# Optimization experiments

Measured on AMD Instinct MI355X. Metric: run time of the kernel, lower is better.

Reference implementation:

```python
import jax, jax.numpy as jnp
import numpy as np

B, T, D_IN, D_H, D_OUT = 32, 2048, 1024, 1024, 1024

def setup_inputs() -> dict:
    key = jax.random.key(0)
    k1, k2, k3, k4, k5 = jax.random.split(key, 5)
    s = jax.random.normal(k1, (B, D_IN), dtype=jnp.float32)
    h = jax.random.normal(k2, (B, T, D_H), dtype=jnp.float32)
    # params (original uses np.random.random, i.e. uniform [0,1); scale kept modest)
    W_a = jax.random.uniform(k3, (D_IN, D_OUT), dtype=jnp.float32)
    U_a = jax.random.uniform(k4, (D_H, D_OUT), dtype=jnp.float32)
    v_a = jax.random.uniform(k5, (D_OUT,), dtype=jnp.float32)
    return {"s": s, "h": h, "W_a": W_a, "U_a": U_a, "v_a": v_a}

def reference(s, h, W_a, U_a, v_a):
    # Bahdanau additive attention:
    # e_bt = v_a . tanh(s W_a + h_t U_a);  a = softmax_t(e);  c_b = sum_t a_bt h_bt
    u_a_h = jnp.einsum('bth,ho->bto', h, U_a)            # [B,T,O]
    w_a_s = jnp.einsum('bi,io->bo', s, W_a)[:, None, :]  # [B,1,O]
    e = jnp.einsum('bto,o->bt', jnp.tanh(w_a_s + u_a_h), v_a)  # [B,T]
    a = jax.nn.softmax(e, axis=-1)                       # [B,T]
    c = jnp.einsum('bt,bth->bh', a, h)                   # [B,H]
    return c
```

## Files before the change

### kernel.cpp

```cpp
#include <hip/hip_runtime.h>
#include <hip/hip_bf16.h>
#include <stdint.h>

#define Bb 32
#define Tt 2048
#define Dd 1024

typedef float    f32x4 __attribute__((ext_vector_type(4)));
typedef _Float16 f16x8 __attribute__((ext_vector_type(8)));
typedef uint32_t u32;

#define WS_E     131072
#define WS_A     393216
#define WS_CP    655360
#define WS_UT    4849664

__device__ __forceinline__ void gll16(const void* g, const void* lds) {
  __builtin_amdgcn_global_load_lds(
      (const __attribute__((address_space(1))) u32*)(uintptr_t)g,
      (__attribute__((address_space(3))) u32*)(uint32_t)(uintptr_t)lds,
      16, 0, 0);
}

__global__ __launch_bounds__(256) void k_ws(const float* __restrict__ s,
                                            const float* __restrict__ W,
                                            float* __restrict__ w_ws) {
  const int b = blockIdx.x >> 2;
  const int o = (blockIdx.x & 3) * 256 + threadIdx.x;
  __shared__ float s_sh[Dd];
#pragma unroll
  for (int j = 0; j < 4; ++j)
    s_sh[threadIdx.x + 256 * j] = s[b * Dd + threadIdx.x + 256 * j];
  __syncthreads();
  float acc = 0.f;
#pragma unroll 8
  for (int i = 0; i < Dd; ++i) acc += s_sh[i] * W[(size_t)i * Dd + o];
  w_ws[b * Dd + o] = acc;
}

__global__ __launch_bounds__(256) void k_ut(const float* __restrict__ U,
                                            uint8_t* __restrict__ U_ts) {
  const int i0 = (blockIdx.x >> 4) * 64;
  const int o0 = (blockIdx.x & 15) * 64;
  __shared__ float tile[64][65];
  const int tx = threadIdx.x & 63;
  const int ty = threadIdx.x >> 6;
#pragma unroll
  for (int jj = 0; jj < 16; ++jj)
    tile[tx][ty + 4 * jj] = U[(size_t)(i0 + ty + 4 * jj) * Dd + o0 + tx];
  __syncthreads();
#pragma unroll
  for (int jj = 0; jj < 16; ++jj) {
    const int o_loc = ty + 4 * jj;
    const int o = o0 + o_loc;
    const int k = i0 + tx;
    const _Float16 hv = (_Float16)tile[o_loc][tx];
    const size_t byte = (size_t)o * 2048 + (((u32)k * 2u) ^ (u32)((o & 7) << 4));
    *(uint16_t*)(U_ts + byte) = *(const uint16_t*)&hv;
  }
}

__global__ __launch_bounds__(256, 2) void k_e(const float* __restrict__ h,
                                              const uint8_t* __restrict__ U_ts,
                                              const float* __restrict__ w_ws,
                                              const float* __restrict__ v_a,
                                              float* __restrict__ e_ws) {
  const int b    = blockIdx.x >> 5;
  const int t0   = (blockIdx.x & 31) << 6;
  const int lane = threadIdx.x & 63;
  const int wv   = threadIdx.x >> 6;

  __shared__ __align__(16) uint8_t ubuf[2][32 * 512];
  __shared__ float w_sh[Dd];
  __shared__ float v_sh[Dd];

#pragma unroll
  for (int j = 0; j < 4; ++j) {
    const int o = threadIdx.x + 256 * j;
    w_sh[o] = w_ws[b * Dd + o];
    v_sh[o] = v_a[o];
  }

  const int trow = t0 + 16 * wv + (lane & 15);
  const int kcol = (lane >> 4) * 8;
  const float* hbase = h + ((size_t)b * Tt + trow) * Dd + kcol;
  f16x8 hreg[32];
#pragma unroll
  for (int ks = 0; ks < 32; ++ks) {
    const f32x4 p0 = *(const f32x4*)(hbase + ks * 32);
    const f32x4 p1 = *(const f32x4*)(hbase + ks * 32 + 4);
    f16x8 r;
    r[0] = (_Float16)p0[0]; r[1] = (_Float16)p0[1];
    r[2] = (_Float16)p0[2]; r[3] = (_Float16)p0[3];
    r[4] = (_Float16)p1[0]; r[5] = (_Float16)p1[1];
    r[6] = (_Float16)p1[2]; r[7] = (_Float16)p1[3];
    hreg[ks] = r;
  }

  auto stage = [&](int c, int buf) {
    const uint8_t* src = U_ts + (size_t)(c >> 2) * (32 * 2048) + (size_t)(c & 3) * 512;
#pragma unroll
    for (int q = 0; q < 4; ++q) {
      const int r0 = 8 * wv + 2 * q;
      gll16(src + (size_t)(r0 + (lane >> 5)) * 2048 + (size_t)(lane & 31) * 16,
            &ubuf[buf][r0 * 512]);
    }
  };

  stage(0, 0);
  __syncthreads();

  float epart = 0.f;
  const int ol0 = lane & 15;
  const int ol1 = ol0 + 16;
  const u32 kb  = (u32)((lane >> 4) * 16);
  const u32 sw  = (u32)((ol0 & 7) << 4);

  for (int ot = 0; ot < 32; ++ot) {
    f32x4 acc0 = {0.f, 0.f, 0.f, 0.f};
    f32x4 acc1 = {0.f, 0.f, 0.f, 0.f};
#pragma unroll
    for (int kc = 0; kc < 4; ++kc) {
      const int c   = ot * 4 + kc;
      const int cur = kc & 1;
      if (c + 1 < 128) stage(c + 1, cur ^ 1);
      const uint8_t* ub = &ubuf[cur][0];
#pragma unroll
      for (int kk = 0; kk < 8; ++kk) {
        const u32 kbyte = (u32)(kk * 64) + kb;
        const f16x8 a0 = *(const f16x8*)(ub + ol0 * 512 + (kbyte ^ sw));
        const f16x8 a1 = *(const f16x8*)(ub + ol1 * 512 + (kbyte ^ sw));
        acc0 = __builtin_amdgcn_mfma_f32_16x16x32_f16(a0, hreg[kc * 8 + kk], acc0, 0, 0, 0);
        acc1 = __builtin_amdgcn_mfma_f32_16x16x32_f16(a1, hreg[kc * 8 + kk], acc1, 0, 0, 0);
      }
      __syncthreads();
    }
    const int ob = (ot << 5) + ((lane >> 4) << 2);
#pragma unroll
    for (int r = 0; r < 4; ++r) {
      const float x0 = acc0[r] + w_sh[ob + r];
      const float x1 = acc1[r] + w_sh[ob + 16 + r];
      epart += v_sh[ob + r]      * (1.f - 2.f / (__expf(2.f * x0) + 1.f));
      epart += v_sh[ob + 16 + r] * (1.f - 2.f / (__expf(2.f * x1) + 1.f));
    }
  }
  epart += __shfl_xor(epart, 16, 64);
  epart += __shfl_xor(epart, 32, 64);
  if (lane < 16) e_ws[b * Tt + t0 + 16 * wv + lane] = epart;
}

__global__ __launch_bounds__(256) void k_sm(const float* __restrict__ e_ws,
                                            float* __restrict__ a_ws) {
  const int b = blockIdx.x;
  const int lane = threadIdx.x & 63;
  const int wv = threadIdx.x >> 6;
  __shared__ float red[8];
  float ev[8];
  float m = -1e30f;
#pragma unroll
  for (int j = 0; j < 8; ++j) {
    ev[j] = e_ws[b * Tt + threadIdx.x + 256 * j];
    m = fmaxf(m, ev[j]);
  }
#pragma unroll
  for (int sft = 1; sft < 64; sft <<= 1) m = fmaxf(m, __shfl_xor(m, sft, 64));
  if (lane == 0) red[wv] = m;
  __syncthreads();
  m = fmaxf(fmaxf(red[0], red[1]), fmaxf(red[2], red[3]));
  float sum = 0.f;
#pragma unroll
  for (int j = 0; j < 8; ++j) { ev[j] = __expf(ev[j] - m); sum += ev[j]; }
#pragma unroll
  for (int sft = 1; sft < 64; sft <<= 1) sum += __shfl_xor(sum, sft, 64);
  if (lane == 0) red[4 + wv] = sum;
  __syncthreads();
  const float inv = 1.f / (red[4] + red[5] + red[6] + red[7]);
#pragma unroll
  for (int j = 0; j < 8; ++j) a_ws[b * Tt + threadIdx.x + 256 * j] = ev[j] * inv;
}

__global__ __launch_bounds__(256) void k_c1(const float* __restrict__ h,
                                            const float* __restrict__ a_ws,
                                            float* __restrict__ cpart) {
  const int b  = blockIdx.x >> 5;
  const int tc = blockIdx.x & 31;
  const int t0 = tc << 6;
  __shared__ float a_sh[64];
  if (threadIdx.x < 64) a_sh[threadIdx.x] = a_ws[b * Tt + t0 + threadIdx.x];
  __syncthreads();
  f32x4 acc = {0.f, 0.f, 0.f, 0.f};
  const float* hb = h + ((size_t)b * Tt + t0) * Dd + threadIdx.x * 4;
#pragma unroll 4
  for (int t = 0; t < 64; ++t) {
    const f32x4 hv = *(const f32x4*)(hb + (size_t)t * Dd);
    acc += a_sh[t] * hv;
  }
  *(f32x4*)(cpart + ((size_t)(tc * 32 + b) << 10) + threadIdx.x * 4) = acc;
}

__global__ __launch_bounds__(256) void k_c2(const float* __restrict__ cpart,
                                            float* __restrict__ out) {
  const int gid = blockIdx.x * 256 + threadIdx.x;
  const int b = gid >> 10;
  const int d = gid & 1023;
  float sv = 0.f;
#pragma unroll
  for (int tc = 0; tc < 32; ++tc) sv += cpart[((size_t)(tc * 32 + b) << 10) + d];
  out[gid] = sv;
}

extern "C" void kernel_launch(void* const* d_in, const int* in_sizes, int n_in,
                              void* d_out, int out_size, void* d_ws, size_t ws_size,
                              hipStream_t stream) {
  (void)in_sizes; (void)n_in; (void)out_size; (void)ws_size;
  const float* s  = (const float*)d_in[0];
  const float* h  = (const float*)d_in[1];
  const float* W  = (const float*)d_in[2];
  const float* U  = (const float*)d_in[3];
  const float* v  = (const float*)d_in[4];
  uint8_t* ws = (uint8_t*)d_ws;
  float*   w_ws  = (float*)ws;
  float*   e_ws  = (float*)(ws + WS_E);
  float*   a_ws  = (float*)(ws + WS_A);
  float*   cpart = (float*)(ws + WS_CP);
  uint8_t* U_ts  = ws + WS_UT;

  k_ws<<<128, 256, 0, stream>>>(s, W, w_ws);
  k_ut<<<256, 256, 0, stream>>>(U, U_ts);
  k_e <<<1024, 256, 0, stream>>>(h, U_ts, w_ws, v, e_ws);
  k_sm<<<Bb, 256, 0, stream>>>(e_ws, a_ws);
  k_c1<<<1024, 256, 0, stream>>>(h, a_ws, cpart);
  k_c2<<<128, 256, 0, stream>>>(cpart, (float*)d_out);
}
```

Baseline: 310.0 us.

## Split K across wave pairs with 2x2 MFMA register tiles and fragment-ordered U layout

Restructures the energy kernel so each wave computes a 2x2 block of MFMA tiles (two output tiles by two time tiles) over half of the K dimension. Partial sums are exchanged between wave pairs through LDS, so each U fragment loaded from LDS feeds two MFMAs. The U transpose kernel now writes U directly in per-lane MFMA fragment order with vectorized stores, and 2*W·s is precomputed to fold into the tanh argument. This cuts LDS reads per MFMA and removes the swizzle address math, at the cost of an extra LDS exchange and barrier per output tile.

```diff
diff --git a/kernel.cpp b/kernel.cpp
--- a/kernel.cpp
+++ b/kernel.cpp
@@ -24,7 +24,7 @@
 
 __global__ __launch_bounds__(256) void k_ws(const float* __restrict__ s,
                                             const float* __restrict__ W,
-                                            float* __restrict__ w_ws) {
+                                            float* __restrict__ w2_ws) {
   const int b = blockIdx.x >> 2;
   const int o = (blockIdx.x & 3) * 256 + threadIdx.x;
   __shared__ float s_sh[Dd];
@@ -35,7 +35,7 @@
   float acc = 0.f;
 #pragma unroll 8
   for (int i = 0; i < Dd; ++i) acc += s_sh[i] * W[(size_t)i * Dd + o];
-  w_ws[b * Dd + o] = acc;
+  w2_ws[b * Dd + o] = 2.f * acc;
 }
 
 __global__ __launch_bounds__(256) void k_ut(const float* __restrict__ U,
@@ -50,103 +50,138 @@
     tile[tx][ty + 4 * jj] = U[(size_t)(i0 + ty + 4 * jj) * Dd + o0 + tx];
   __syncthreads();
 #pragma unroll
-  for (int jj = 0; jj < 16; ++jj) {
-    const int o_loc = ty + 4 * jj;
+  for (int it = 0; it < 2; ++it) {
+    const int g = it * 256 + threadIdx.x;
+    const int o_loc = g & 63;
+    const int kg = g >> 6;
     const int o = o0 + o_loc;
-    const int k = i0 + tx;
-    const _Float16 hv = (_Float16)tile[o_loc][tx];
-    const size_t byte = (size_t)o * 2048 + (((u32)k * 2u) ^ (u32)((o & 7) << 4));
-    *(uint16_t*)(U_ts + byte) = *(const uint16_t*)&hv;
+    const int k = i0 + kg * 8;
+    f16x8 r;
+#pragma unroll
+    for (int m = 0; m < 8; ++m) r[m] = (_Float16)tile[o_loc][kg * 8 + m];
+    const int c    = (o >> 5) * 4 + (k >> 8);
+    const int kk   = (k >> 5) & 7;
+    const int half = (o >> 4) & 1;
+    const int ln   = ((k >> 3) & 3) * 16 + (o & 15);
+    *(f16x8*)(U_ts + (size_t)c * 16384 + kk * 2048 + half * 1024 + ln * 16) = r;
   }
 }
 
 __global__ __launch_bounds__(256, 2) void k_e(const float* __restrict__ h,
                                               const uint8_t* __restrict__ U_ts,
-                                              const float* __restrict__ w_ws,
+                                              const float* __restrict__ w2_ws,
                                               const float* __restrict__ v_a,
                                               float* __restrict__ e_ws) {
   const int b    = blockIdx.x >> 5;
   const int t0   = (blockIdx.x & 31) << 6;
   const int lane = threadIdx.x & 63;
   const int wv   = threadIdx.x >> 6;
-
-  __shared__ __align__(16) uint8_t ubuf[2][32 * 512];
-  __shared__ float w_sh[Dd];
-  __shared__ float v_sh[Dd];
-
-#pragma unroll
-  for (int j = 0; j < 4; ++j) {
-    const int o = threadIdx.x + 256 * j;
-    w_sh[o] = w_ws[b * Dd + o];
-    v_sh[o] = v_a[o];
-  }
-
-  const int trow = t0 + 16 * wv + (lane & 15);
-  const int kcol = (lane >> 4) * 8;
-  const float* hbase = h + ((size_t)b * Tt + trow) * Dd + kcol;
+  const int kh   = wv & 1;
+  const int th   = wv >> 1;
+
+  __shared__ __align__(16) uint8_t ubuf[2][16384];
+  __shared__ __align__(16) float   exch[2048];
+
   f16x8 hreg[32];
-#pragma unroll
-  for (int ks = 0; ks < 32; ++ks) {
-    const f32x4 p0 = *(const f32x4*)(hbase + ks * 32);
-    const f32x4 p1 = *(const f32x4*)(hbase + ks * 32 + 4);
-    f16x8 r;
-    r[0] = (_Float16)p0[0]; r[1] = (_Float16)p0[1];
-    r[2] = (_Float16)p0[2]; r[3] = (_Float16)p0[3];
-    r[4] = (_Float16)p1[0]; r[5] = (_Float16)p1[1];
-    r[6] = (_Float16)p1[2]; r[7] = (_Float16)p1[3];
-    hreg[ks] = r;
+  {
+    const int tcol = t0 + th * 32 + (lane & 15);
+    const int kgrp = (lane >> 4) * 8;
+    const float* hb0 = h + ((size_t)b * Tt + tcol) * Dd;
+    const float* hb1 = hb0 + (size_t)16 * Dd;
+#pragma unroll
+    for (int ss = 0; ss < 16; ++ss) {
+      const int kbase = (ss >> 2) * 256 + kh * 128 + (ss & 3) * 32 + kgrp;
+      f32x4 p0 = *(const f32x4*)(hb0 + kbase);
+      f32x4 p1 = *(const f32x4*)(hb0 + kbase + 4);
+      f16x8 r;
+      r[0] = (_Float16)p0[0]; r[1] = (_Float16)p0[1];
+      r[2] = (_Float16)p0[2]; r[3] = (_Float16)p0[3];
+      r[4] = (_Float16)p1[0]; r[5] = (_Float16)p1[1];
+      r[6] = (_Float16)p1[2]; r[7] = (_Float16)p1[3];
+      hreg[ss * 2] = r;
+      p0 = *(const f32x4*)(hb1 + kbase);
+      p1 = *(const f32x4*)(hb1 + kbase + 4);
+      r[0] = (_Float16)p0[0]; r[1] = (_Float16)p0[1];
+      r[2] = (_Float16)p0[2]; r[3] = (_Float16)p0[3];
+      r[4] = (_Float16)p1[0]; r[5] = (_Float16)p1[1];
+      r[6] = (_Float16)p1[2]; r[7] = (_Float16)p1[3];
+      hreg[ss * 2 + 1] = r;
+    }
   }
 
   auto stage = [&](int c, int buf) {
-    const uint8_t* src = U_ts + (size_t)(c >> 2) * (32 * 2048) + (size_t)(c & 3) * 512;
-#pragma unroll
-    for (int q = 0; q < 4; ++q) {
-      const int r0 = 8 * wv + 2 * q;
-      gll16(src + (size_t)(r0 + (lane >> 5)) * 2048 + (size_t)(lane & 31) * 16,
-            &ubuf[buf][r0 * 512]);
-    }
+    const uint8_t* src = U_ts + (size_t)c * 16384 + (size_t)(wv * 4) * 1024 + (size_t)lane * 16;
+#pragma unroll
+    for (int q = 0; q < 4; ++q)
+      gll16(src + q * 1024, &ubuf[buf][(wv * 4 + q) * 1024]);
   };
 
   stage(0, 0);
   __syncthreads();
 
-  float epart = 0.f;
-  const int ol0 = lane & 15;
-  const int ol1 = ol0 + 16;
-  const u32 kb  = (u32)((lane >> 4) * 16);
-  const u32 sw  = (u32)((ol0 & 7) << 4);
+  float ep0 = 0.f, ep1 = 0.f;
+  const float* wp  = w2_ws + b * Dd;
+  const int    obl = kh * 16 + ((lane >> 4) << 2);
 
   for (int ot = 0; ot < 32; ++ot) {
-    f32x4 acc0 = {0.f, 0.f, 0.f, 0.f};
-    f32x4 acc1 = {0.f, 0.f, 0.f, 0.f};
+    const f32x4 w4 = *(const f32x4*)(wp + (ot << 5) + obl);
+    const f32x4 v4 = *(const f32x4*)(v_a + (ot << 5) + obl);
+    f32x4 accA0 = {0.f,0.f,0.f,0.f}, accA1 = {0.f,0.f,0.f,0.f};
+    f32x4 accB0 = {0.f,0.f,0.f,0.f}, accB1 = {0.f,0.f,0.f,0.f};
 #pragma unroll
     for (int kc = 0; kc < 4; ++kc) {
       const int c   = ot * 4 + kc;
       const int cur = kc & 1;
       if (c + 1 < 128) stage(c + 1, cur ^ 1);
-      const uint8_t* ub = &ubuf[cur][0];
-#pragma unroll
-      for (int kk = 0; kk < 8; ++kk) {
-        const u32 kbyte = (u32)(kk * 64) + kb;
-        const f16x8 a0 = *(const f16x8*)(ub + ol0 * 512 + (kbyte ^ sw));
-        const f16x8 a1 = *(const f16x8*)(ub + ol1 * 512 + (kbyte ^ sw));
-        acc0 = __builtin_amdgcn_mfma_f32_16x16x32_f16(a0, hreg[kc * 8 + kk], acc0, 0, 0, 0);
-        acc1 = __builtin_amdgcn_mfma_f32_16x16x32_f16(a1, hreg[kc * 8 + kk], acc1, 0, 0, 0);
+      const uint8_t* ub = &ubuf[cur][0] + kh * 8192 + lane * 16;
+#pragma unroll
+      for (int kkl = 0; kkl < 4; ++kkl) {
+        const f16x8 a0 = *(const f16x8*)(ub + kkl * 2048);
+        const f16x8 a1 = *(const f16x8*)(ub + kkl * 2048 + 1024);
+        const f16x8 b0 = hreg[(kc * 4 + kkl) * 2];
+        const f16x8 b1 = hreg[(kc * 4 + kkl) * 2 + 1];
+        accA0 = __builtin_amdgcn_mfma_f32_16x16x32_f16(a0, b0, accA0, 0, 0, 0);
+        accA1 = __builtin_amdgcn_mfma_f32_16x16x32_f16(a0, b1, accA1, 0, 0, 0);
+        accB0 = __builtin_amdgcn_mfma_f32_16x16x32_f16(a1, b0, accB0, 0, 0, 0);
+        accB1 = __builtin_amdgcn_mfma_f32_16x16x32_f16(a1, b1, accB1, 0, 0, 0);
       }
       __syncthreads();
     }
-    const int ob = (ot << 5) + ((lane >> 4) << 2);
-#pragma unroll
-    for (int r = 0; r < 4; ++r) {
-      const float x0 = acc0[r] + w_sh[ob + r];
-      const float x1 = acc1[r] + w_sh[ob + 16 + r];
-      epart += v_sh[ob + r]      * (1.f - 2.f / (__expf(2.f * x0) + 1.f));
-      epart += v_sh[ob + 16 + r] * (1.f - 2.f / (__expf(2.f * x1) + 1.f));
-    }
-  }
-  epart += __shfl_xor(epart, 16, 64);
-  epart += __shfl_xor(epart, 32, 64);
-  if (lane < 16) e_ws[b * Tt + t0 + 16 * wv + lane] = epart;
+    {
+      float* snd = exch + wv * 512 + lane * 4;
+      if (kh == 0) { *(f32x4*)snd = accB0; *(f32x4*)(snd + 256) = accB1; }
+      else         { *(f32x4*)snd = accA0; *(f32x4*)(snd + 256) = accA1; }
+    }
+    __syncthreads();
+    {
+      const float* rcv = exch + (wv ^ 1) * 512 + lane * 4;
+      const f32x4 q0 = *(const f32x4*)rcv;
+      const f32x4 q1 = *(const f32x4*)(rcv + 256);
+      f32x4 x0, x1;
+      if (kh == 0) { x0 = accA0 + q0; x1 = accA1 + q1; }
+      else         { x0 = accB0 + q0; x1 = accB1 + q1; }
+#pragma unroll
+      for (int r = 0; r < 4; ++r) {
+        const float e0 = __expf(__builtin_fmaf(x0[r], 2.f, w4[r]));
+        const float e1 = __expf(__builtin_fmaf(x1[r], 2.f, w4[r]));
+        ep0 += v4[r] * (1.f - 2.f / (e0 + 1.f));
+        ep1 += v4[r] * (1.f - 2.f / (e1 + 1.f));
+      }
+    }
+  }
+
+  ep0 += __shfl_xor(ep0, 16, 64); ep0 += __shfl_xor(ep0, 32, 64);
+  ep1 += __shfl_xor(ep1, 16, 64); ep1 += __shfl_xor(ep1, 32, 64);
+  __syncthreads();
+  if (kh == 1 && lane < 16) {
+    exch[th * 32 + lane]      = ep0;
+    exch[th * 32 + 16 + lane] = ep1;
+  }
+  __syncthreads();
+  if (kh == 0 && lane < 16) {
+    e_ws[b * Tt + t0 + th * 32 + lane]      = ep0 + exch[th * 32 + lane];
+    e_ws[b * Tt + t0 + th * 32 + 16 + lane] = ep1 + exch[th * 32 + 16 + lane];
+  }
 }
 
 __global__ __launch_bounds__(256) void k_sm(const float* __restrict__ e_ws,
@@ -219,15 +254,15 @@
   const float* U  = (const float*)d_in[3];
   const float* v  = (const float*)d_in[4];
   uint8_t* ws = (uint8_t*)d_ws;
-  float*   w_ws  = (float*)ws;
+  float*   w2_ws = (float*)ws;
   float*   e_ws  = (float*)(ws + WS_E);
   float*   a_ws  = (float*)(ws + WS_A);
   float*   cpart = (float*)(ws + WS_CP);
   uint8_t* U_ts  = ws + WS_UT;
 
-  k_ws<<<128, 256, 0, stream>>>(s, W, w_ws);
+  k_ws<<<128, 256, 0, stream>>>(s, W, w2_ws);
   k_ut<<<256, 256, 0, stream>>>(U, U_ts);
-  k_e <<<1024, 256, 0, stream>>>(h, U_ts, w_ws, v, e_ws);
+  k_e <<<1024, 256, 0, stream>>>(h, U_ts, w2_ws, v, e_ws);
   k_sm<<<Bb, 256, 0, stream>>>(e_ws, a_ws);
   k_c1<<<1024, 256, 0, stream>>>(h, a_ws, cpart);
   k_c2<<<128, 256, 0, stream>>>(cpart, (float*)d_out);
```

New measurement: 306.8 us. No clear change (-1.0%).
